# Kernel optimization log

Measured on AMD Instinct MI355X. Metric: run time of the kernel, lower is better.

## Reference

```python
import jax, jax.numpy as jnp
import numpy as np

N_NODES = 50000
N_EDGES = 400000
F_IN = 128
HID = 64
HEADS = 8
N_CLASSES = 16
NEG_SLOPE = 0.2  # PyG GATConv default negative_slope


def _glorot(key, shape):
    fan_in, fan_out = shape[0], shape[-1]
    lim = jnp.sqrt(6.0 / (fan_in + fan_out))
    return jax.random.uniform(key, shape, jnp.float32, -lim, lim)


def setup_inputs() -> dict:
    key = jax.random.key(0)
    ks = jax.random.split(key, 16)
    x = jax.random.normal(ks[0], (N_NODES, F_IN), jnp.float32)
    edge_index = jax.random.randint(ks[1], (2, N_EDGES), 0, N_NODES, jnp.int64)
    # layer 0: F_IN -> HEADS*HID (concat)
    W0 = _glorot(ks[2], (F_IN, HEADS * HID))
    a_s0 = _glorot(ks[3], (HEADS, HID))
    a_d0 = _glorot(ks[4], (HEADS, HID))
    b0 = jnp.zeros((HEADS * HID,), jnp.float32)
    # layer 1: HEADS*HID -> HEADS*HID (concat)
    W1 = _glorot(ks[5], (HEADS * HID, HEADS * HID))
    a_s1 = _glorot(ks[6], (HEADS, HID))
    a_d1 = _glorot(ks[7], (HEADS, HID))
    b1 = jnp.zeros((HEADS * HID,), jnp.float32)
    # final layer: HEADS*HID -> N_CLASSES, heads=1, concat=False (mean over heads)
    W2 = _glorot(ks[8], (HEADS * HID, 1 * N_CLASSES))
    a_s2 = _glorot(ks[9], (1, N_CLASSES))
    a_d2 = _glorot(ks[10], (1, N_CLASSES))
    b2 = jnp.zeros((N_CLASSES,), jnp.float32)
    return {"x": x, "edge_index": edge_index,
            "W0": W0, "a_s0": a_s0, "a_d0": a_d0, "b0": b0,
            "W1": W1, "a_s1": a_s1, "a_d1": a_d1, "b1": b1,
            "W2": W2, "a_s2": a_s2, "a_d2": a_d2, "b2": b2}


def gat_conv(x, src, dst, W, a_src, a_dst, b, num_nodes, concat):
    """One PyG-style GATConv (self-loops already in src/dst).
    x: [N, F_in]; W: [F_in, H*C]; a_src/a_dst: [H, C]; b: [H*C] or [C]."""
    H, C = a_src.shape
    h = (x @ W).reshape(num_nodes, H, C)                    # [N,H,C]
    al_s = jnp.einsum('nhc,hc->nh', h, a_src)               # [N,H]
    al_d = jnp.einsum('nhc,hc->nh', h, a_dst)               # [N,H]
    e = jax.nn.leaky_relu(al_s[src] + al_d[dst], NEG_SLOPE) # [E,H]
    # scatter-softmax over incoming edges of each destination node
    m = jax.ops.segment_max(e, dst, num_segments=num_nodes)  # [N,H]
    ex = jnp.exp(e - m[dst])
    denom = jax.ops.segment_sum(ex, dst, num_segments=num_nodes)
    alpha = ex / denom[dst]                                  # [E,H]
    out = jax.ops.segment_sum(alpha[:, :, None] * h[src], dst,
                              num_segments=num_nodes)        # [N,H,C]
    if concat:
        return out.reshape(num_nodes, H * C) + b
    return out.mean(axis=1) + b


def reference(x, edge_index, W0, a_s0, a_d0, b0, W1, a_s1, a_d1, b1,
              W2, a_s2, a_d2, b2):
    N = x.shape[0]
    # PyG GATConv adds self-loops by default
    loops = jnp.arange(N, dtype=edge_index.dtype)
    src = jnp.concatenate([edge_index[0], loops])
    dst = jnp.concatenate([edge_index[1], loops])
    h = gat_conv(x, src, dst, W0, a_s0, a_d0, b0, N, concat=True)
    h = jax.nn.elu(h)  # dropout is identity in eval mode
    h = gat_conv(h, src, dst, W1, a_s1, a_d1, b1, N, concat=True)
    h = jax.nn.elu(h)
    return gat_conv(h, src, dst, W2, a_s2, a_d2, b2, N, concat=False)
```

## Files before the change

### kernel.cpp

```cpp
#include <hip/hip_runtime.h>

#define N_NODES 50000
#define N_EDGES 400000
#define E_TOT   450000
#define NEG 0.2f
#define NB_SCAN ((N_NODES + 255) / 256)
#define MAXD 64

typedef unsigned short ushort_t;
typedef __attribute__((ext_vector_type(8))) _Float16 half8;
typedef __attribute__((ext_vector_type(4))) float  f32x4;
typedef __attribute__((ext_vector_type(8))) unsigned short ushort8;

__device__ __forceinline__ ushort_t f2h(float f){
    _Float16 h = (_Float16)f;
    union { _Float16 h; ushort_t u; } v; v.h = h; return v.u;
}
__device__ __forceinline__ float h_lo(unsigned u){
    union { unsigned u; _Float16 h[2]; } v; v.u = u; return (float)v.h[0];
}
__device__ __forceinline__ float h_hi(unsigned u){
    union { unsigned u; _Float16 h[2]; } v; v.u = u; return (float)v.h[1];
}
__device__ __forceinline__ void gload_lds16(const void* g, void* l){
    __builtin_amdgcn_global_load_lds((const __attribute__((address_space(1))) void*)g,
                                     (__attribute__((address_space(3))) void*)l, 16, 0, 0);
}
__device__ __forceinline__ int wave_incl_scan(int v, int lane){
    #pragma unroll
    for(int off = 1; off < 64; off <<= 1){
        int t = __shfl_up(v, off, 64);
        if(lane >= off) v += t;
    }
    return v;
}


__global__ void cvt_all(const float* __restrict__ W0,
                        const float* __restrict__ W1, const float* __restrict__ W2,
                        const int* __restrict__ ei,
                        ushort_t* __restrict__ W0t,
                        ushort_t* __restrict__ W1t, ushort_t* __restrict__ W2t,
                        int* __restrict__ deg){
    int i = blockIdx.x*256 + threadIdx.x;
    if(i < 512*128){ int n = i >> 7, k = i & 127; W0t[i] = f2h(W0[(size_t)k*512 + n]); }
    if(i < 512*512){ int n = i >> 9, k = i & 511; W1t[i] = f2h(W1[(size_t)k*512 + n]); }
    if(i < 16*512){ int n = i >> 9, k = i & 511; W2t[i] = f2h(W2[(size_t)k*16 + n]); }
    if(i < E_TOT){
        int dst = (i < N_EDGES) ? ei[N_EDGES + i] : (i - N_EDGES);
        atomicAdd(&deg[dst], 1);
    }
}


__global__ void deg_block_sum(const int* __restrict__ deg, int* __restrict__ bsum){
    int i = blockIdx.x*256 + threadIdx.x;
    int lane = threadIdx.x & 63, wave = threadIdx.x >> 6;
    int v = (i < N_NODES) ? deg[i] : 0;
    #pragma unroll
    for(int off = 1; off < 64; off <<= 1) v += __shfl_xor(v, off, 64);
    __shared__ int sw[4];
    if(lane == 0) sw[wave] = v;
    __syncthreads();
    if(threadIdx.x == 0) bsum[blockIdx.x] = sw[0] + sw[1] + sw[2] + sw[3];
}

__global__ void scan_apply(const int* __restrict__ bsum,
                           int* __restrict__ dw, int* __restrict__ rowptr){
    __shared__ int soff;
    __shared__ int sw[4];
    int i = blockIdx.x*256 + threadIdx.x;
    int lane = threadIdx.x & 63, wave = threadIdx.x >> 6;
    if(wave == 0){
        int s = 0;
        for(int j = lane; j < (int)blockIdx.x; j += 64) s += bsum[j];
        #pragma unroll
        for(int off = 1; off < 64; off <<= 1) s += __shfl_xor(s, off, 64);
        if(lane == 0) soff = s;
    }
    int v = (i < N_NODES) ? dw[i] : 0;
    int incl = wave_incl_scan(v, lane);
    if(lane == 63) sw[wave] = incl;
    __syncthreads();
    int add = soff;
    for(int w = 0; w < wave; w++) add += sw[w];
    int excl = incl - v + add;
    if(i < N_NODES){ rowptr[i] = excl; dw[i] = excl; }
    if(i == N_NODES-1) rowptr[N_NODES] = excl + v;
}

__global__ void scatter_edges(const int* __restrict__ ei, int* __restrict__ wofs,
                              int* __restrict__ csr){
    int e = blockIdx.x*256 + threadIdx.x;
    if(e >= E_TOT) return;
    int src, dst;
    if(e < N_EDGES){ src = ei[e]; dst = ei[N_EDGES + e]; }
    else { src = dst = e - N_EDGES; }
    int pos = atomicAdd(&wofs[dst], 1);
    csr[pos] = src;
}


__global__ __launch_bounds__(256) void gemm_l0(const float* __restrict__ A,
                                               const ushort_t* __restrict__ Bt,
                                               ushort_t* __restrict__ Cb,
                                               const float* __restrict__ a_s,
                                               const float* __restrict__ a_d,
                                               float* __restrict__ als,
                                               float* __restrict__ ald, int M){
    extern __shared__ ushort_t lds[];
    ushort_t* As = lds;
    ushort_t* Bs = lds + 128*128;
    int tid = threadIdx.x, wave = tid >> 6, lane = tid & 63;
    int wm = wave & 1, wn = wave >> 1;
    int row0 = blockIdx.y * 128;
    int col0 = blockIdx.x * 128;

    {
        int rsub = lane >> 4;
        int c16  = lane & 15;
        #pragma unroll
        for(int i = 0; i < 8; i++){
            int rl = wave*32 + i*4 + rsub;
            int br = col0 + rl;
            int sc = c16 ^ (rl & 7);
            gload_lds16(Bt + (size_t)br*128 + sc*8, Bs + (wave*32 + i*4)*128);
        }
    }

    {
        int rsub = lane >> 4;
        int c16  = lane & 15;
        #pragma unroll
        for(int j = 0; j < 8; j++){
            int rl = wave*32 + j*4 + rsub;
            int gr = row0 + rl; gr = gr < M ? gr : M-1;
            const float* ap = A + (size_t)gr*128 + c16*8;
            f32x4 lo = *(const f32x4*)ap;
            f32x4 hi = *(const f32x4*)(ap + 4);
            union { _Float16 h[8]; half8 v; } u;
            u.h[0] = (_Float16)lo[0]; u.h[1] = (_Float16)lo[1];
            u.h[2] = (_Float16)lo[2]; u.h[3] = (_Float16)lo[3];
            u.h[4] = (_Float16)hi[0]; u.h[5] = (_Float16)hi[1];
            u.h[6] = (_Float16)hi[2]; u.h[7] = (_Float16)hi[3];
            int dc = c16 ^ (rl & 7);
            *(half8*)&As[(size_t)rl*128 + dc*8] = u.v;
        }
    }

    __syncthreads();

    f32x4 acc[4][4] = {};
    int fm = lane & 15, fq = lane >> 4;
    #pragma unroll
    for(int kt = 0; kt < 4; kt++){
        half8 a[4], b[4];
        #pragma unroll
        for(int t = 0; t < 4; t++){
            int ra = wm*64 + t*16 + fm;
            a[t] = *(const half8*)&As[ra*128 + (((kt*4 + fq) ^ (ra & 7)))*8];
            int rb = wn*64 + t*16 + fm;
            b[t] = *(const half8*)&Bs[rb*128 + (((kt*4 + fq) ^ (rb & 7)))*8];
        }
        #pragma unroll
        for(int i = 0; i < 4; i++)
            #pragma unroll
            for(int j = 0; j < 4; j++)
                acc[i][j] = __builtin_amdgcn_mfma_f32_16x16x32_f16(a[i], b[j], acc[i][j], 0, 0, 0);
    }

    int cm = (lane >> 4) * 4, cn = lane & 15;
    int head = (col0 + wn*64) >> 6;
    float as_[4], ad_[4];
    #pragma unroll
    for(int j = 0; j < 4; j++){
        int c = head*64 + cn + j*16;
        as_[j] = a_s[c]; ad_[j] = a_d[c];
    }
    #pragma unroll
    for(int i = 0; i < 4; i++){
        #pragma unroll
        for(int p = 0; p < 4; p++){
            int r = row0 + wm*64 + i*16 + cm + p;
            float ps = 0.f, pd = 0.f;
            if(r < M){
                ushort_t* cp = &Cb[(size_t)r*512 + col0 + wn*64 + cn];
                #pragma unroll
                for(int j = 0; j < 4; j++){
                    float v = acc[i][j][p];
                    cp[j*16] = f2h(v);
                    ps += v*as_[j]; pd += v*ad_[j];
                }
            }
            #pragma unroll
            for(int off = 1; off < 16; off <<= 1){
                ps += __shfl_xor(ps, off);
                pd += __shfl_xor(pd, off);
            }
            if(cn == 0 && r < M){ als[r*8 + head] = ps; ald[r*8 + head] = pd; }
        }
    }
}


template<int K>
__global__ __launch_bounds__(512, 2) void gemm_bt8(const ushort_t* __restrict__ A,
                                                   const ushort_t* __restrict__ Bt,
                                                   ushort_t* __restrict__ Cb,
                                                   const float* __restrict__ a_s,
                                                   const float* __restrict__ a_d,
                                                   float* __restrict__ als,
                                                   float* __restrict__ ald, int M){
    extern __shared__ ushort_t lds[];
    constexpr int NT = K / 64;
    int tid = threadIdx.x, wave = tid >> 6, lane = tid & 63;
    int wm = wave >> 2, wn = wave & 3;

    int s = blockIdx.x, nb = gridDim.x;
    int cc = s & 7, kk = s >> 3;
    int q = nb >> 3, rr = nb & 7;
    int t = (cc < rr ? cc*(q+1) : rr*(q+1) + (cc-rr)*q) + kk;
    int row0 = (t >> 1) * 256;
    int col0 = (t & 1) * 256;

    int lr = lane >> 3;
    int cs8 = ((lane & 7) ^ lr) << 3;
    int arows[4], brows[4];
    #pragma unroll
    for(int i = 0; i < 4; i++){
        int r = row0 + (wave << 5) + (i << 3) + lr;
        arows[i] = r < M ? r : M-1;
        brows[i] = col0 + (wave << 5) + (i << 3) + lr;
    }

    int l15 = lane & 15, fq = lane >> 4;
    int xr = (lane & 7) << 4;
    int xco0 = ((fq << 4)      ) ^ xr;
    int xco1 = (64 | (fq << 4)) ^ xr;

    f32x4 acc[8][4] = {};

    auto stage = [&](int nbuf, int kt, int i){
        ushort_t* la = lds + nbuf*16384 + (wave << 11) + (i << 9);
        ushort_t* lb = lds + 32768 + nbuf*16384 + (wave << 11) + (i << 9);
        gload_lds16(A  + (size_t)arows[i]*K + kt + cs8, la);
        gload_lds16(Bt + (size_t)brows[i]*K + kt + cs8, lb);
    };

    #pragma unroll
    for(int i = 0; i < 4; i++) stage(0, 0, i);

    for(int it = 0; it < NT; ++it){
        int b = it & 1;
        asm volatile("s_waitcnt vmcnt(0)" ::: "memory");
        __builtin_amdgcn_s_barrier();
        const char* Ac = (const char*)(lds + b*16384);
        const char* Bc = (const char*)(lds + 32768 + b*16384);
        #pragma unroll
        for(int p = 0; p < 4; ++p){
            if(it < NT-1 && p < 2){
                stage(b ^ 1, (it + 1) << 6, 2*p);
                stage(b ^ 1, (it + 1) << 6, 2*p + 1);
            }
            half8 aF[2][2], bF[4][2];
            #pragma unroll
            for(int m2 = 0; m2 < 2; m2++){
                int ro = (((wm << 7) + (((p << 1) | m2) << 4) + l15)) << 7;
                aF[m2][0] = *(const half8*)(Ac + ro + xco0);
                aF[m2][1] = *(const half8*)(Ac + ro + xco1);
            }
            #pragma unroll
            for(int nj = 0; nj < 4; nj++){
                int ro = (((wn << 6) + (nj << 4) + l15)) << 7;
                bF[nj][0] = *(const half8*)(Bc + ro + xco0);
                bF[nj][1] = *(const half8*)(Bc + ro + xco1);
            }
            __builtin_amdgcn_s_barrier();
            __builtin_amdgcn_s_setprio(1);
            #pragma unroll
            for(int m2 = 0; m2 < 2; m2++)
                #pragma unroll
                for(int nj = 0; nj < 4; nj++){
                    acc[(p<<1)|m2][nj] = __builtin_amdgcn_mfma_f32_16x16x32_f16(aF[m2][0], bF[nj][0], acc[(p<<1)|m2][nj], 0, 0, 0);
                    acc[(p<<1)|m2][nj] = __builtin_amdgcn_mfma_f32_16x16x32_f16(aF[m2][1], bF[nj][1], acc[(p<<1)|m2][nj], 0, 0, 0);
                }
            __builtin_amdgcn_s_setprio(0);
            __builtin_amdgcn_s_barrier();
        }
    }

    int head = (col0 >> 6) + wn;
    float asv[4], adv[4];
    #pragma unroll
    for(int nj = 0; nj < 4; nj++){
        int c = (head << 6) + (nj << 4) + l15;
        asv[nj] = a_s[c]; adv[nj] = a_d[c];
    }
    #pragma unroll
    for(int mi = 0; mi < 8; mi++){
        #pragma unroll
        for(int p2 = 0; p2 < 4; p2++){
            int r = row0 + (wm << 7) + (mi << 4) + (fq << 2) + p2;
            float ps = 0.f, pd = 0.f;
            if(r < M){
                ushort_t* cp = &Cb[(size_t)r*512 + (head << 6) + l15];
                #pragma unroll
                for(int nj = 0; nj < 4; nj++){
                    float v = acc[mi][nj][p2];
                    cp[nj << 4] = f2h(v);
                    ps += v*asv[nj]; pd += v*adv[nj];
                }
            }
            #pragma unroll
            for(int off = 1; off < 16; off <<= 1){
                ps += __shfl_xor(ps, off);
                pd += __shfl_xor(pd, off);
            }
            if(l15 == 0 && r < M){ als[r*8 + head] = ps; ald[r*8 + head] = pd; }
        }
    }
}


__global__ __launch_bounds__(256) void attn_agg(const ushort_t* __restrict__ h,
        const float* __restrict__ als, const float* __restrict__ ald,
        const int* __restrict__ rowptr, const int* __restrict__ csr,
        const float* __restrict__ bias, ushort_t* __restrict__ out){
    __shared__ float sm[4][8], sd[4][8];
    __shared__ float sex[4][MAXD][8];
    int wv = threadIdx.x >> 6, lane = threadIdx.x & 63;
    int n = blockIdx.x*4 + wv;
    int start = rowptr[n], end = rowptr[n+1];

    int hd = lane & 7, e8 = lane >> 3;
    float aldv = ald[n*8 + hd];
    float lmax = -1e30f;
    for(int idx = start + e8; idx < end; idx += 8){
        int e = idx - start;
        int src = csr[idx];
        float v = als[src*8 + hd] + aldv;
        v = v > 0.f ? v : NEG*v;
        if(e < MAXD) sex[wv][e][hd] = v;
        lmax = fmaxf(lmax, v);
    }
    for(int off = 8; off < 64; off <<= 1) lmax = fmaxf(lmax, __shfl_xor(lmax, off));
    float lsum = 0.f;
    for(int idx = start + e8; idx < end; idx += 8){
        int e = idx - start;
        float v;
        if(e < MAXD) v = sex[wv][e][hd];
        else { int src = csr[idx]; v = als[src*8 + hd] + aldv; v = v > 0.f ? v : NEG*v; }
        float ex = __expf(v - lmax);
        if(e < MAXD) sex[wv][e][hd] = ex;
        lsum += ex;
    }
    for(int off = 8; off < 64; off <<= 1) lsum += __shfl_xor(lsum, off);
    if(lane < 8){ sm[wv][hd] = lmax; sd[wv][hd] = 1.f / lsum; }
    __syncthreads();

    int head = lane >> 3;
    float inv = sd[wv][head];
    float acc[8] = {};

    int cnt = end - start;
    int nmain = cnt < MAXD ? cnt : MAXD;
    int mend = start + nmain;
    int last = mend - 1;
    for(int idx = start; idx < mend; idx += 8){
        int ss[8]; uint4 pp[8]; float ee[8];
        #pragma unroll
        for(int k = 0; k < 8; k++){
            int j = idx + k;
            ss[k] = csr[j <= last ? j : last];
        }
        #pragma unroll
        for(int k = 0; k < 8; k++)
            pp[k] = *(const uint4*)&h[(size_t)ss[k]*512 + lane*8];
        #pragma unroll
        for(int k = 0; k < 8; k++){
            int j = idx + k;
            ee[k] = (j < mend) ? sex[wv][j-start][head] : 0.f;
        }
        #pragma unroll
        for(int k = 0; k < 8; k++){
            acc[0] += ee[k]*h_lo(pp[k].x); acc[1] += ee[k]*h_hi(pp[k].x);
            acc[2] += ee[k]*h_lo(pp[k].y); acc[3] += ee[k]*h_hi(pp[k].y);
            acc[4] += ee[k]*h_lo(pp[k].z); acc[5] += ee[k]*h_hi(pp[k].z);
            acc[6] += ee[k]*h_lo(pp[k].w); acc[7] += ee[k]*h_hi(pp[k].w);
        }
    }
    if(mend < end){
        float m = sm[wv][head];
        float aldn = ald[n*8 + head];
        for(int idx = mend; idx < end; idx++){
            int src = csr[idx];
            float v = als[src*8 + head] + aldn;
            v = v > 0.f ? v : NEG*v;
            float e0 = __expf(v - m);
            uint4 p = *(const uint4*)&h[(size_t)src*512 + lane*8];
            acc[0] += e0*h_lo(p.x); acc[1] += e0*h_hi(p.x);
            acc[2] += e0*h_lo(p.y); acc[3] += e0*h_hi(p.y);
            acc[4] += e0*h_lo(p.z); acc[5] += e0*h_hi(p.z);
            acc[6] += e0*h_lo(p.w); acc[7] += e0*h_hi(p.w);
        }
    }

    ushort8 o;
    #pragma unroll
    for(int j = 0; j < 8; j++){
        float v = acc[j]*inv + bias[lane*8 + j];
        v = v > 0.f ? v : (__expf(v) - 1.f);
        o[j] = f2h(v);
    }
    *(ushort8*)&out[(size_t)n*512 + lane*8] = o;
}


__global__ __launch_bounds__(256) void gemm2_mfma(const ushort_t* __restrict__ A,
                                                  const ushort_t* __restrict__ W2t,
                                                  const float* __restrict__ a_s2,
                                                  const float* __restrict__ a_d2,
                                                  float* __restrict__ C,
                                                  float* __restrict__ als,
                                                  float* __restrict__ ald){
    int wave = threadIdx.x >> 6, lane = threadIdx.x & 63;
    long row0 = (long)(blockIdx.x*4 + wave)*16;
    int fr = lane & 15, fq = lane >> 4;
    long ar = row0 + fr;
    if(ar > N_NODES-1) ar = N_NODES-1;
    const ushort_t* ap = A + ar*512 + fq*8;
    const ushort_t* bp = W2t + (size_t)fr*512 + fq*8;
    f32x4 acc = {};
    #pragma unroll
    for(int kt = 0; kt < 512; kt += 32){
        half8 a = *(const half8*)(ap + kt);
        half8 b = *(const half8*)(bp + kt);
        acc = __builtin_amdgcn_mfma_f32_16x16x32_f16(a, b, acc, 0, 0, 0);
    }
    float as_ = a_s2[fr], ad_ = a_d2[fr];
    #pragma unroll
    for(int p = 0; p < 4; p++){
        long r = row0 + fq*4 + p;
        float v = acc[p];
        float ps = v*as_, pd = v*ad_;
        #pragma unroll
        for(int off = 1; off < 16; off <<= 1){
            ps += __shfl_xor(ps, off);
            pd += __shfl_xor(pd, off);
        }
        if(r < N_NODES){
            C[r*16 + fr] = v;
            if(fr == 0){ als[r] = ps; ald[r] = pd; }
        }
    }
}

__global__ __launch_bounds__(256) void attn_agg2(const float* __restrict__ h2,
        const float* __restrict__ als, const float* __restrict__ ald,
        const int* __restrict__ rowptr, const int* __restrict__ csr,
        const float* __restrict__ b2, float* __restrict__ out){
    __shared__ float sex2[16][MAXD+1];
    int wv = threadIdx.x >> 6, lane = threadIdx.x & 63;
    int q = lane >> 4, c = lane & 15;
    int slot = wv*4 + q;
    int n = blockIdx.x*16 + slot;
    int start = rowptr[n], end = rowptr[n+1];
    float aldv = ald[n];
    int cnt = end - start;
    int nmain = cnt < MAXD ? cnt : MAXD;
    int mend = start + nmain;

    float lmax = -1e30f;
    for(int idx = start + c; idx < end; idx += 16){
        int e = idx - start;
        float v = als[csr[idx]] + aldv; v = v > 0.f ? v : NEG*v;
        if(e < MAXD) sex2[slot][e] = v;
        lmax = fmaxf(lmax, v);
    }
    #pragma unroll
    for(int off = 1; off < 16; off <<= 1) lmax = fmaxf(lmax, __shfl_xor(lmax, off));
    float lsum = 0.f;
    for(int idx = start + c; idx < end; idx += 16){
        int e = idx - start;
        float v;
        if(e < MAXD) v = sex2[slot][e];
        else { v = als[csr[idx]] + aldv; v = v > 0.f ? v : NEG*v; }
        float ex = __expf(v - lmax);
        if(e < MAXD) sex2[slot][e] = ex;
        lsum += ex;
    }
    #pragma unroll
    for(int off = 1; off < 16; off <<= 1) lsum += __shfl_xor(lsum, off);
    float inv = 1.f / lsum;

    float acc = 0.f;
    for(int idx = start; idx < mend; idx++){
        int src = csr[idx];
        float ex = sex2[slot][idx - start];
        acc += ex * h2[(size_t)src*16 + c];
    }
    for(int idx = mend; idx < end; idx++){
        int src = csr[idx];
        float v = als[src] + aldv; v = v > 0.f ? v : NEG*v;
        acc += __expf(v - lmax) * h2[(size_t)src*16 + c];
    }
    out[(size_t)n*16 + c] = acc*inv + b2[c];
}


extern "C" void kernel_launch(void* const* d_in, const int* in_sizes, int n_in,
                              void* d_out, int out_size, void* d_ws, size_t ws_size,
                              hipStream_t stream) {
    const float* x    = (const float*)d_in[0];
    const int*   ei   = (const int*)  d_in[1];
    const float* W0   = (const float*)d_in[2];
    const float* a_s0 = (const float*)d_in[3];
    const float* a_d0 = (const float*)d_in[4];
    const float* b0   = (const float*)d_in[5];
    const float* W1   = (const float*)d_in[6];
    const float* a_s1 = (const float*)d_in[7];
    const float* a_d1 = (const float*)d_in[8];
    const float* b1   = (const float*)d_in[9];
    const float* W2   = (const float*)d_in[10];
    const float* a_s2 = (const float*)d_in[11];
    const float* a_d2 = (const float*)d_in[12];
    const float* b2   = (const float*)d_in[13];
    float* out = (float*)d_out;

    char* w = (char*)d_ws;
    auto alloc = [&](size_t bytes){ void* p = (void*)w; w += (bytes + 255) & ~(size_t)255; return p; };
    int*      rowptr = (int*)     alloc((N_NODES+1)*sizeof(int));
    int*      wofs   = (int*)     alloc((N_NODES+1)*sizeof(int));
    int*      bsum   = (int*)     alloc(NB_SCAN*sizeof(int));
    int*      csr    = (int*)     alloc(E_TOT*sizeof(int));
    float*    als    = (float*)   alloc((size_t)N_NODES*8*sizeof(float));
    float*    ald    = (float*)   alloc((size_t)N_NODES*8*sizeof(float));
    float*    als2   = (float*)   alloc((size_t)N_NODES*sizeof(float));
    float*    ald2   = (float*)   alloc((size_t)N_NODES*sizeof(float));
    ushort_t* hb     = (ushort_t*)alloc((size_t)N_NODES*512*sizeof(ushort_t));
    ushort_t* hbf    = (ushort_t*)alloc((size_t)N_NODES*512*sizeof(ushort_t));
    ushort_t* W0t    = (ushort_t*)alloc((size_t)512*128*sizeof(ushort_t));
    ushort_t* W1t    = (ushort_t*)alloc((size_t)512*512*sizeof(ushort_t));
    ushort_t* W2t    = (ushort_t*)alloc((size_t)16*512*sizeof(ushort_t));
    float*    h2     = (float*)   alloc((size_t)N_NODES*16*sizeof(float));

    const int NBLK = 2 * ((N_NODES + 255) / 256);

    (void)hipFuncSetAttribute((const void*)gemm_bt8<512>,
                              hipFuncAttributeMaxDynamicSharedMemorySize, 131072);
    (void)hipFuncSetAttribute((const void*)gemm_l0,
                              hipFuncAttributeMaxDynamicSharedMemorySize, 65536);

    hipMemsetAsync(wofs, 0, (N_NODES+1)*sizeof(int), stream);
    cvt_all<<<(E_TOT+255)/256, 256, 0, stream>>>(W0, W1, W2, ei, W0t, W1t, W2t, wofs);

    deg_block_sum<<<NB_SCAN, 256, 0, stream>>>(wofs, bsum);
    scan_apply<<<NB_SCAN, 256, 0, stream>>>(bsum, wofs, rowptr);
    scatter_edges<<<(E_TOT+255)/256, 256, 0, stream>>>(ei, wofs, csr);

    gemm_l0<<<dim3(4, (N_NODES+127)/128), 256, 65536, stream>>>(x, W0t, hb, a_s0, a_d0, als, ald, N_NODES);
    attn_agg<<<N_NODES/4, 256, 0, stream>>>(hb, als, ald, rowptr, csr, b0, hbf);

    gemm_bt8<512><<<NBLK, 512, 131072, stream>>>(hbf, W1t, hb, a_s1, a_d1, als, ald, N_NODES);
    attn_agg<<<N_NODES/4, 256, 0, stream>>>(hb, als, ald, rowptr, csr, b1, hbf);

    gemm2_mfma<<<(N_NODES+63)/64, 256, 0, stream>>>(hbf, W2t, a_s2, a_d2, h2, als2, ald2);
    attn_agg2<<<N_NODES/16, 256, 0, stream>>>(h2, als2, ald2, rowptr, csr, b2, out);
}
```

Before: 429.3 us.

## Restructure layer-0 GEMM to full-width tiles, deepen GEMM prefetch, drop agg sync

The layer-0 GEMM now has each 512-thread block compute all 512 output columns for 128 rows, so x is read and converted to fp16 once per row tile instead of four times. Each wave owns one head, and the full transposed weight is kept in a large LDS buffer. The layer-1 GEMM now prefetches two K-tiles ahead, using partial vmcnt waits and issuing the next loads after the fragment reads, to overlap global loads with MFMA work. The attention aggregation replaces a shared-memory exchange and __syncthreads with wave shuffles. The trade-offs are the large LDS footprint limiting occupancy in the layer-0 GEMM and tighter wait-count ordering in the pipeline.

New measurement: 419.5 us. -2.3%, faster.

```diff
diff --git a/kernel.cpp b/kernel.cpp
--- a/kernel.cpp
+++ b/kernel.cpp
@@ -101,41 +101,36 @@
 }
 
 
-__global__ __launch_bounds__(256) void gemm_l0(const float* __restrict__ A,
-                                               const ushort_t* __restrict__ Bt,
-                                               ushort_t* __restrict__ Cb,
-                                               const float* __restrict__ a_s,
-                                               const float* __restrict__ a_d,
-                                               float* __restrict__ als,
-                                               float* __restrict__ ald, int M){
+__global__ __launch_bounds__(512, 2) void gemm0f(const float* __restrict__ x,
+                                                 const ushort_t* __restrict__ W0t,
+                                                 ushort_t* __restrict__ Cb,
+                                                 const float* __restrict__ a_s,
+                                                 const float* __restrict__ a_d,
+                                                 float* __restrict__ als,
+                                                 float* __restrict__ ald, int M){
     extern __shared__ ushort_t lds[];
     ushort_t* As = lds;
     ushort_t* Bs = lds + 128*128;
     int tid = threadIdx.x, wave = tid >> 6, lane = tid & 63;
-    int wm = wave & 1, wn = wave >> 1;
-    int row0 = blockIdx.y * 128;
-    int col0 = blockIdx.x * 128;
+    int row0 = blockIdx.x * 128;
 
     {
-        int rsub = lane >> 4;
-        int c16  = lane & 15;
-        #pragma unroll
-        for(int i = 0; i < 8; i++){
-            int rl = wave*32 + i*4 + rsub;
-            int br = col0 + rl;
-            int sc = c16 ^ (rl & 7);
-            gload_lds16(Bt + (size_t)br*128 + sc*8, Bs + (wave*32 + i*4)*128);
-        }
-    }
-
+        int rsub = lane >> 4, c16 = lane & 15;
+        #pragma unroll
+        for(int s = 0; s < 16; s++){
+            int rowq = wave*64 + s*4;
+            int r = rowq + rsub;
+            int sc = c16 ^ (r & 7);
+            gload_lds16(W0t + (size_t)r*128 + sc*8, Bs + rowq*128);
+        }
+    }
     {
-        int rsub = lane >> 4;
-        int c16  = lane & 15;
-        #pragma unroll
-        for(int j = 0; j < 8; j++){
-            int rl = wave*32 + j*4 + rsub;
+        int rsub = lane >> 4, c16 = lane & 15;
+        #pragma unroll
+        for(int t = 0; t < 4; t++){
+            int rl = wave*16 + t*4 + rsub;
             int gr = row0 + rl; gr = gr < M ? gr : M-1;
-            const float* ap = A + (size_t)gr*128 + c16*8;
+            const float* ap = x + (size_t)gr*128 + c16*8;
             f32x4 lo = *(const f32x4*)ap;
             f32x4 hi = *(const f32x4*)(ap + 4);
             union { _Float16 h[8]; half8 v; } u;
@@ -143,53 +138,54 @@
             u.h[2] = (_Float16)lo[2]; u.h[3] = (_Float16)lo[3];
             u.h[4] = (_Float16)hi[0]; u.h[5] = (_Float16)hi[1];
             u.h[6] = (_Float16)hi[2]; u.h[7] = (_Float16)hi[3];
-            int dc = c16 ^ (rl & 7);
-            *(half8*)&As[(size_t)rl*128 + dc*8] = u.v;
+            *(half8*)&As[(size_t)rl*128 + (c16 ^ (rl & 7))*8] = u.v;
         }
     }
 
     __syncthreads();
 
-    f32x4 acc[4][4] = {};
+    f32x4 acc[8][4] = {};
     int fm = lane & 15, fq = lane >> 4;
     #pragma unroll
     for(int kt = 0; kt < 4; kt++){
-        half8 a[4], b[4];
-        #pragma unroll
-        for(int t = 0; t < 4; t++){
-            int ra = wm*64 + t*16 + fm;
-            a[t] = *(const half8*)&As[ra*128 + (((kt*4 + fq) ^ (ra & 7)))*8];
-            int rb = wn*64 + t*16 + fm;
-            b[t] = *(const half8*)&Bs[rb*128 + (((kt*4 + fq) ^ (rb & 7)))*8];
-        }
-        #pragma unroll
-        for(int i = 0; i < 4; i++)
+        half8 a[8], b[4];
+        #pragma unroll
+        for(int mi = 0; mi < 8; mi++){
+            int r = mi*16 + fm;
+            a[mi] = *(const half8*)&As[(size_t)r*128 + ((kt*4 + fq) ^ (r & 7))*8];
+        }
+        #pragma unroll
+        for(int nj = 0; nj < 4; nj++){
+            int r = wave*64 + nj*16 + fm;
+            b[nj] = *(const half8*)&Bs[(size_t)r*128 + ((kt*4 + fq) ^ (r & 7))*8];
+        }
+        #pragma unroll
+        for(int mi = 0; mi < 8; mi++)
             #pragma unroll
-            for(int j = 0; j < 4; j++)
-                acc[i][j] = __builtin_amdgcn_mfma_f32_16x16x32_f16(a[i], b[j], acc[i][j], 0, 0, 0);
-    }
-
-    int cm = (lane >> 4) * 4, cn = lane & 15;
-    int head = (col0 + wn*64) >> 6;
-    float as_[4], ad_[4];
-    #pragma unroll
-    for(int j = 0; j < 4; j++){
-        int c = head*64 + cn + j*16;
-        as_[j] = a_s[c]; ad_[j] = a_d[c];
-    }
-    #pragma unroll
-    for(int i = 0; i < 4; i++){
-        #pragma unroll
-        for(int p = 0; p < 4; p++){
-            int r = row0 + wm*64 + i*16 + cm + p;
+            for(int nj = 0; nj < 4; nj++)
+                acc[mi][nj] = __builtin_amdgcn_mfma_f32_16x16x32_f16(a[mi], b[nj], acc[mi][nj], 0, 0, 0);
+    }
+
+    int head = wave;
+    float asv[4], adv[4];
+    #pragma unroll
+    for(int nj = 0; nj < 4; nj++){
+        int c = head*64 + nj*16 + fm;
+        asv[nj] = a_s[c]; adv[nj] = a_d[c];
+    }
+    #pragma unroll
+    for(int mi = 0; mi < 8; mi++){
+        #pragma unroll
+        for(int p2 = 0; p2 < 4; p2++){
+            int r = row0 + mi*16 + fq*4 + p2;
             float ps = 0.f, pd = 0.f;
             if(r < M){
-                ushort_t* cp = &Cb[(size_t)r*512 + col0 + wn*64 + cn];
+                ushort_t* cp = &Cb[(size_t)r*512 + head*64 + fm];
                 #pragma unroll
-                for(int j = 0; j < 4; j++){
-                    float v = acc[i][j][p];
-                    cp[j*16] = f2h(v);
-                    ps += v*as_[j]; pd += v*ad_[j];
+                for(int nj = 0; nj < 4; nj++){
+                    float v = acc[mi][nj][p2];
+                    cp[nj*16] = f2h(v);
+                    ps += v*asv[nj]; pd += v*adv[nj];
                 }
             }
             #pragma unroll
@@ -197,7 +193,7 @@
                 ps += __shfl_xor(ps, off);
                 pd += __shfl_xor(pd, off);
             }
-            if(cn == 0 && r < M){ als[r*8 + head] = ps; ald[r*8 + head] = pd; }
+            if(fm == 0 && r < M){ als[r*8 + head] = ps; ald[r*8 + head] = pd; }
         }
     }
 }
@@ -249,19 +245,18 @@
 
     #pragma unroll
     for(int i = 0; i < 4; i++) stage(0, 0, i);
+    #pragma unroll
+    for(int i = 0; i < 4; i++) stage(1, 64, i);
 
     for(int it = 0; it < NT; ++it){
         int b = it & 1;
-        asm volatile("s_waitcnt vmcnt(0)" ::: "memory");
+        if(it < NT-1) asm volatile("s_waitcnt vmcnt(8)" ::: "memory");
+        else         asm volatile("s_waitcnt vmcnt(0)" ::: "memory");
         __builtin_amdgcn_s_barrier();
         const char* Ac = (const char*)(lds + b*16384);
         const char* Bc = (const char*)(lds + 32768 + b*16384);
         #pragma unroll
         for(int p = 0; p < 4; ++p){
-            if(it < NT-1 && p < 2){
-                stage(b ^ 1, (it + 1) << 6, 2*p);
-                stage(b ^ 1, (it + 1) << 6, 2*p + 1);
-            }
             half8 aF[2][2], bF[4][2];
             #pragma unroll
             for(int m2 = 0; m2 < 2; m2++){
@@ -275,7 +270,12 @@
                 bF[nj][0] = *(const half8*)(Bc + ro + xco0);
                 bF[nj][1] = *(const half8*)(Bc + ro + xco1);
             }
+            if(p == 3) asm volatile("s_waitcnt lgkmcnt(0)" ::: "memory");
             __builtin_amdgcn_s_barrier();
+            if(p == 3 && it < NT-2){
+                #pragma unroll
+                for(int i = 0; i < 4; i++) stage(b, (it + 2) << 6, i);
+            }
             __builtin_amdgcn_s_setprio(1);
             #pragma unroll
             for(int m2 = 0; m2 < 2; m2++)
@@ -326,7 +326,6 @@
         const float* __restrict__ als, const float* __restrict__ ald,
         const int* __restrict__ rowptr, const int* __restrict__ csr,
         const float* __restrict__ bias, ushort_t* __restrict__ out){
-    __shared__ float sm[4][8], sd[4][8];
     __shared__ float sex[4][MAXD][8];
     int wv = threadIdx.x >> 6, lane = threadIdx.x & 63;
     int n = blockIdx.x*4 + wv;
@@ -355,11 +354,12 @@
         lsum += ex;
     }
     for(int off = 8; off < 64; off <<= 1) lsum += __shfl_xor(lsum, off);
-    if(lane < 8){ sm[wv][hd] = lmax; sd[wv][hd] = 1.f / lsum; }
-    __syncthreads();
-
-    int head = lane >> 3;
-    float inv = sd[wv][head];
+
+    int head = e8;
+    float m_all = __shfl(lmax, head);
+    float inv   = 1.f / __shfl(lsum, head);
+    float aldn  = __shfl(aldv, head);
+
     float acc[8] = {};
 
     int cnt = end - start;
@@ -390,13 +390,11 @@
         }
     }
     if(mend < end){
-        float m = sm[wv][head];
-        float aldn = ald[n*8 + head];
         for(int idx = mend; idx < end; idx++){
             int src = csr[idx];
             float v = als[src*8 + head] + aldn;
             v = v > 0.f ? v : NEG*v;
-            float e0 = __expf(v - m);
+            float e0 = __expf(v - m_all);
             uint4 p = *(const uint4*)&h[(size_t)src*512 + lane*8];
             acc[0] += e0*h_lo(p.x); acc[1] += e0*h_hi(p.x);
             acc[2] += e0*h_lo(p.y); acc[3] += e0*h_hi(p.y);
@@ -545,11 +543,12 @@
     float*    h2     = (float*)   alloc((size_t)N_NODES*16*sizeof(float));
 
     const int NBLK = 2 * ((N_NODES + 255) / 256);
+    const int NG0  = (N_NODES + 127) / 128;
 
     (void)hipFuncSetAttribute((const void*)gemm_bt8<512>,
                               hipFuncAttributeMaxDynamicSharedMemorySize, 131072);
-    (void)hipFuncSetAttribute((const void*)gemm_l0,
-                              hipFuncAttributeMaxDynamicSharedMemorySize, 65536);
+    (void)hipFuncSetAttribute((const void*)gemm0f,
+                              hipFuncAttributeMaxDynamicSharedMemorySize, 163840);
 
     hipMemsetAsync(wofs, 0, (N_NODES+1)*sizeof(int), stream);
     cvt_all<<<(E_TOT+255)/256, 256, 0, stream>>>(W0, W1, W2, ei, W0t, W1t, W2t, wofs);
@@ -558,7 +557,7 @@
     scan_apply<<<NB_SCAN, 256, 0, stream>>>(bsum, wofs, rowptr);
     scatter_edges<<<(E_TOT+255)/256, 256, 0, stream>>>(ei, wofs, csr);
 
-    gemm_l0<<<dim3(4, (N_NODES+127)/128), 256, 65536, stream>>>(x, W0t, hb, a_s0, a_d0, als, ald, N_NODES);
+    gemm0f<<<NG0, 512, 163840, stream>>>(x, W0t, hb, a_s0, a_d0, als, ald, N_NODES);
     attn_agg<<<N_NODES/4, 256, 0, stream>>>(hb, als, ald, rowptr, csr, b0, hbf);
 
     gemm_bt8<512><<<NBLK, 512, 131072, stream>>>(hbf, W1t, hb, a_s1, a_d1, als, ald, N_NODES);
```
